# Optimization experiments

Hardware: AMD Instinct MI355X
Metric: run time of the kernel (lower is better)

The kernel has to match this reference:

```python
import jax, jax.numpy as jnp
import numpy as np
from jax import lax

PS = 8  # patch size

def setup_inputs() -> dict:
    key = jax.random.key(0)
    ks = jax.random.split(key, 7)
    dim = 64
    B, H, W = 4, 256, 256
    x = jax.random.normal(ks[0], (B, dim, H, W), dtype=jnp.float32)
    # to_hidden: Conv2d(dim, 6*dim, k=1)
    w_hidden = jax.random.normal(ks[1], (6 * dim, dim, 1, 1), dtype=jnp.float32) * 0.05
    b_hidden = jax.random.normal(ks[2], (6 * dim,), dtype=jnp.float32) * 0.01
    # to_hidden_dw: depthwise Conv2d(6*dim, 6*dim, k=3, pad=1, groups=6*dim)
    w_dw = jax.random.normal(ks[3], (6 * dim, 1, 3, 3), dtype=jnp.float32) * 0.05
    b_dw = jax.random.normal(ks[4], (6 * dim,), dtype=jnp.float32) * 0.01
    # project_out: Conv2d(2*dim, dim, k=1)
    w_out = jax.random.normal(ks[5], (dim, 2 * dim, 1, 1), dtype=jnp.float32) * 0.05
    b_out = jax.random.normal(ks[6], (dim,), dtype=jnp.float32) * 0.01
    return {"x": x, "w_hidden": w_hidden, "b_hidden": b_hidden,
            "w_dw": w_dw, "b_dw": b_dw, "w_out": w_out, "b_out": b_out}

def _conv(x, w, groups=1, padding='VALID'):
    return lax.conv_general_dilated(
        x, w, window_strides=(1, 1), padding=padding,
        dimension_numbers=('NCHW', 'OIHW', 'NCHW'),
        feature_group_count=groups)

def reference(x, w_hidden, b_hidden, w_dw, b_dw, w_out, b_out):
    # 1x1 expansion to 6*dim channels
    hidden = _conv(x, w_hidden) + b_hidden[None, :, None, None]
    # 3x3 depthwise conv (groups == channels)
    dw = _conv(hidden, w_dw, groups=w_dw.shape[0], padding='SAME') + b_dw[None, :, None, None]
    q, k, v = jnp.split(dw, 3, axis=1)  # each (B, 2*dim, H, W)
    B, C, H, W = q.shape
    # raw reshape into (B,C,H/8,W/8,8,8) exactly as torch .reshape on contiguous NCHW
    q_patch = q.reshape(B, C, H // PS, W // PS, PS, PS)
    k_patch = k.reshape(B, C, H // PS, W // PS, PS, PS)
    q_fft = jnp.fft.rfft2(q_patch)
    k_fft = jnp.fft.rfft2(k_patch)
    out = jnp.fft.irfft2(q_fft * k_fft, s=(PS, PS))  # circular conv of q,k patches
    out = out.reshape(B, C, (H // PS) * PS, (W // PS) * PS)
    output = v * out
    output = _conv(output, w_out) + b_out[None, :, None, None]
    return output
```

## Files before the change

kernel.cpp:

```cpp
#include <hip/hip_runtime.h>

#define HW 65536
#define W_IMG 256
#define H_IMG 256
#define CIN 64
#define CHID 384
#define CQK 128

__global__ __launch_bounds__(256) void k1_expand(
    const float* __restrict__ x_base,
    const float* __restrict__ wh,
    const float* __restrict__ bh,
    float* __restrict__ hidden_base,
    size_t x_bstride, size_t hid_bstride)
{
    const float* x = x_base + blockIdx.z * x_bstride;
    float* hidden  = hidden_base + blockIdx.z * hid_bstride;
    const int pxbase = blockIdx.x * 256;
    const int cobase = blockIdx.y * 48;
    const int tid  = threadIdx.x;
    const int lane = tid & 63;
    const int wq   = __builtin_amdgcn_readfirstlane(tid >> 6);
    const int px   = pxbase + lane * 4;
    const int cw   = cobase + wq * 12;

    float acc[12][4];
    #pragma unroll
    for (int i = 0; i < 12; ++i)
        #pragma unroll
        for (int j = 0; j < 4; ++j) acc[i][j] = 0.f;

    #pragma unroll 2
    for (int ci4 = 0; ci4 < CIN; ci4 += 4) {
        float4 xv[4];
        #pragma unroll
        for (int u = 0; u < 4; ++u)
            xv[u] = *reinterpret_cast<const float4*>(&x[(size_t)(ci4 + u) * HW + px]);
        #pragma unroll
        for (int i = 0; i < 12; ++i) {
            float4 wv = *reinterpret_cast<const float4*>(
                &wh[(size_t)(cw + i) * CIN + ci4]);
            float wu[4] = {wv.x, wv.y, wv.z, wv.w};
            #pragma unroll
            for (int u = 0; u < 4; ++u) {
                acc[i][0] += wu[u] * xv[u].x;
                acc[i][1] += wu[u] * xv[u].y;
                acc[i][2] += wu[u] * xv[u].z;
                acc[i][3] += wu[u] * xv[u].w;
            }
        }
    }

    #pragma unroll
    for (int i = 0; i < 12; ++i) {
        int co = cw + i;
        float b = bh[co];
        float4 o;
        o.x = acc[i][0] + b; o.y = acc[i][1] + b;
        o.z = acc[i][2] + b; o.w = acc[i][3] + b;
        *reinterpret_cast<float4*>(&hidden[(size_t)co * HW + px]) = o;
    }
}

#define QK_CH   2208
#define QK_ROW  276
#define QK_SEG  68
__global__ __launch_bounds__(256) void k2_fused(
    const float* __restrict__ hidden_base,
    const float* __restrict__ wdw,
    const float* __restrict__ bdw,
    float* __restrict__ vout_base,
    size_t hid_bstride, size_t vout_bstride)
{
    __shared__ float stg[10 * 264];
    __shared__ float qk[2 * QK_CH];

    const float* hidden = hidden_base + blockIdx.z * hid_bstride;
    float* vout         = vout_base + blockIdx.z * vout_bstride;

    const int c  = blockIdx.y;
    const int r0 = blockIdx.x * 8;
    const int tid = threadIdx.x;

    const int row = tid >> 5;
    const int seg = (tid >> 3) & 3;
    const int i   = tid & 7;
    const int gr  = r0 + row;
    const int wp0 = seg * 64 + i * 8;

    const float* hbv = hidden + (size_t)(c + 2 * CQK) * HW;
    float4 hv[3][2];
    float  hm[3], hp[3];
    #pragma unroll
    for (int ky = 0; ky < 3; ++ky) {
        int grr = gr + ky - 1;
        hv[ky][0] = make_float4(0.f, 0.f, 0.f, 0.f);
        hv[ky][1] = make_float4(0.f, 0.f, 0.f, 0.f);
        hm[ky] = 0.f; hp[ky] = 0.f;
        if ((unsigned)grr < H_IMG) {
            const float* rb = hbv + (size_t)grr * W_IMG;
            hv[ky][0] = *reinterpret_cast<const float4*>(&rb[wp0]);
            hv[ky][1] = *reinterpret_cast<const float4*>(&rb[wp0 + 4]);
            hm[ky] = (wp0 > 0)   ? rb[wp0 - 1] : 0.f;
            hp[ky] = (wp0 < 248) ? rb[wp0 + 8] : 0.f;
        }
    }

    const int w = tid;
    const int segw = w >> 6;
    const int tw   = w & 63;

    #pragma unroll
    for (int ch = 0; ch < 2; ++ch) {
        if (ch) __syncthreads();
        #pragma unroll
        for (int it = 0; it < 3; ++it) {
            int f4 = it * 256 + tid;
            if (f4 < 640) {
                int lr = f4 >> 6;
                int p4 = f4 & 63;
                int grr = r0 - 1 + lr;
                float4 v = make_float4(0.f, 0.f, 0.f, 0.f);
                if ((unsigned)grr < H_IMG)
                    v = *reinterpret_cast<const float4*>(
                        &hidden[(size_t)(c + ch * CQK) * HW + (size_t)grr * W_IMG + p4 * 4]);
                *reinterpret_cast<float4*>(&stg[lr * 264 + 4 + p4 * 4]) = v;
            }
        }
        if (tid < 10) {
            stg[tid * 264 + 3]   = 0.f;
            stg[tid * 264 + 260] = 0.f;
        }
        __syncthreads();

        const float* wv = wdw + (c + ch * CQK) * 9;
        const float bias = bdw[c + ch * CQK];
        const float w0 = wv[0], w1 = wv[1], w2 = wv[2];
        const float w3 = wv[3], w4 = wv[4], w5 = wv[5];
        const float w6 = wv[6], w7 = wv[7], w8 = wv[8];

        const float* S0 = &stg[w + 3];
        float am = S0[0],       a0 = S0[1],       ap = S0[2];
        float bm = S0[264],     b0 = S0[265],     bp = S0[266];
        #pragma unroll
        for (int r = 0; r < 8; ++r) {
            const float* Sr = S0 + (r + 2) * 264;
            float cm = Sr[0], c0 = Sr[1], cp = Sr[2];
            float a = bias + am * w0 + a0 * w1 + ap * w2
                           + bm * w3 + b0 * w4 + bp * w5
                           + cm * w6 + c0 * w7 + cp * w8;
            qk[ch * QK_CH + r * QK_ROW + segw * QK_SEG + tw] = a;
            am = bm; a0 = b0; ap = bp;
            bm = cm; b0 = c0; bp = cp;
        }
    }
    __syncthreads();

    const float* qb = &qk[row * QK_ROW + seg * QK_SEG];
    const float* kb = &qk[QK_CH + row * QK_ROW + seg * QK_SEG];

    float acc[8];
    #pragma unroll
    for (int j = 0; j < 8; ++j) acc[j] = 0.f;

    #pragma unroll
    for (int s = 0; s < 8; ++s) {
        int qr = (i - s) & 7;
        float4 ka = *reinterpret_cast<const float4*>(&kb[s * 8]);
        float4 kc = *reinterpret_cast<const float4*>(&kb[s * 8 + 4]);
        float4 qa = *reinterpret_cast<const float4*>(&qb[qr * 8]);
        float4 qc = *reinterpret_cast<const float4*>(&qb[qr * 8 + 4]);
        float kr[8] = {ka.x, ka.y, ka.z, ka.w, kc.x, kc.y, kc.z, kc.w};
        float qv[8] = {qa.x, qa.y, qa.z, qa.w, qc.x, qc.y, qc.z, qc.w};
        #pragma unroll
        for (int t = 0; t < 8; ++t)
            #pragma unroll
            for (int j = 0; j < 8; ++j)
                acc[j] += kr[t] * qv[(j - t) & 7];
    }

    const float* wvv = wdw + (c + 2 * CQK) * 9;
    const float vbias = bdw[c + 2 * CQK];
    float vc[8];
    #pragma unroll
    for (int j = 0; j < 8; ++j) vc[j] = vbias;
    #pragma unroll
    for (int ky = 0; ky < 3; ++ky) {
        float kw0 = wvv[ky * 3], kw1 = wvv[ky * 3 + 1], kw2 = wvv[ky * 3 + 2];
        float h[10];
        h[0] = hm[ky];
        h[1] = hv[ky][0].x; h[2] = hv[ky][0].y; h[3] = hv[ky][0].z; h[4] = hv[ky][0].w;
        h[5] = hv[ky][1].x; h[6] = hv[ky][1].y; h[7] = hv[ky][1].z; h[8] = hv[ky][1].w;
        h[9] = hp[ky];
        #pragma unroll
        for (int j = 0; j < 8; ++j)
            vc[j] += h[j] * kw0 + h[j + 1] * kw1 + h[j + 2] * kw2;
    }

    float* dst = &vout[(size_t)c * HW + (size_t)gr * W_IMG + wp0];
    float4 o0, o1;
    o0.x = acc[0] * vc[0]; o0.y = acc[1] * vc[1];
    o0.z = acc[2] * vc[2]; o0.w = acc[3] * vc[3];
    o1.x = acc[4] * vc[4]; o1.y = acc[5] * vc[5];
    o1.z = acc[6] * vc[6]; o1.w = acc[7] * vc[7];
    *reinterpret_cast<float4*>(dst)     = o0;
    *reinterpret_cast<float4*>(dst + 4) = o1;
}

__global__ __launch_bounds__(256) void k3_project(
    const float* __restrict__ vout_base,
    const float* __restrict__ wo,
    const float* __restrict__ bo,
    float* __restrict__ out_base,
    size_t vout_bstride, size_t out_bstride)
{
    const float* vout = vout_base + blockIdx.z * vout_bstride;
    float* out        = out_base + blockIdx.z * out_bstride;
    const int pxbase = blockIdx.x * 256;
    const int cobase = blockIdx.y * 16;
    const int tid  = threadIdx.x;
    const int lane = tid & 63;
    const int wq   = __builtin_amdgcn_readfirstlane(tid >> 6);
    const int px   = pxbase + lane * 4;
    const int cw   = cobase + wq * 4;

    float acc[4][4];
    #pragma unroll
    for (int i = 0; i < 4; ++i)
        #pragma unroll
        for (int j = 0; j < 4; ++j) acc[i][j] = 0.f;

    #pragma unroll 2
    for (int cc4 = 0; cc4 < CQK; cc4 += 4) {
        float4 xv[4];
        #pragma unroll
        for (int u = 0; u < 4; ++u)
            xv[u] = *reinterpret_cast<const float4*>(&vout[(size_t)(cc4 + u) * HW + px]);
        #pragma unroll
        for (int i = 0; i < 4; ++i) {
            float4 wv = *reinterpret_cast<const float4*>(
                &wo[(size_t)(cw + i) * CQK + cc4]);
            float wu[4] = {wv.x, wv.y, wv.z, wv.w};
            #pragma unroll
            for (int u = 0; u < 4; ++u) {
                acc[i][0] += wu[u] * xv[u].x;
                acc[i][1] += wu[u] * xv[u].y;
                acc[i][2] += wu[u] * xv[u].z;
                acc[i][3] += wu[u] * xv[u].w;
            }
        }
    }

    #pragma unroll
    for (int i = 0; i < 4; ++i) {
        int co = cw + i;
        float b = bo[co];
        float4 o;
        o.x = acc[i][0] + b; o.y = acc[i][1] + b;
        o.z = acc[i][2] + b; o.w = acc[i][3] + b;
        *reinterpret_cast<float4*>(&out[(size_t)co * HW + px]) = o;
    }
}

extern "C" void kernel_launch(void* const* d_in, const int* in_sizes, int n_in,
                              void* d_out, int out_size, void* d_ws, size_t ws_size,
                              hipStream_t stream) {
    const float* x   = (const float*)d_in[0];
    const float* wh  = (const float*)d_in[1];
    const float* bh  = (const float*)d_in[2];
    const float* wdw = (const float*)d_in[3];
    const float* bdw = (const float*)d_in[4];
    const float* wo  = (const float*)d_in[5];
    const float* bo  = (const float*)d_in[6];
    float* out = (float*)d_out;

    const size_t n_hid  = (size_t)CHID * HW;
    const size_t n_vout = (size_t)CQK * HW;
    const size_t n_x    = (size_t)CIN * HW;

    if (ws_size >= 4 * (n_hid + n_vout) * sizeof(float)) {
        float* hidden = (float*)d_ws;
        float* vout   = hidden + 4 * n_hid;
        k1_expand <<<dim3(HW / 256, CHID / 48, 4), 256, 0, stream>>>(
            x, wh, bh, hidden, n_x, n_hid);
        k2_fused  <<<dim3(H_IMG / 8, CQK, 4),      256, 0, stream>>>(
            hidden, wdw, bdw, vout, n_hid, n_vout);
        k3_project<<<dim3(HW / 256, 64 / 16, 4),   256, 0, stream>>>(
            vout, wo, bo, out, n_vout, n_x);
    } else {
        float* hidden = (float*)d_ws;
        float* vout   = hidden + n_hid;
        for (int b = 0; b < 4; ++b) {
            const float* xb = x + (size_t)b * n_x;
            float* ob       = out + (size_t)b * n_x;
            k1_expand <<<dim3(HW / 256, CHID / 48, 1), 256, 0, stream>>>(
                xb, wh, bh, hidden, 0, 0);
            k2_fused  <<<dim3(H_IMG / 8, CQK, 1),      256, 0, stream>>>(
                hidden, wdw, bdw, vout, 0, 0);
            k3_project<<<dim3(HW / 256, 64 / 16, 1),   256, 0, stream>>>(
                vout, wo, bo, ob, 0, 0);
        }
    }
}
```

Measured before the change: 403.8 us.

## Prefetch q/k tiles into registers upfront and split expand into two passes

In the fused depthwise/FFT kernel, the q and k halo tiles are now loaded from global memory into registers at kernel start, before the v loads, so all global reads are in flight together. The second channel's tile is then written to shared memory from registers instead of being fetched after a barrier. The expand kernel now computes its 12 output channels per wave as two passes of 6, which lowers accumulator register pressure but reloads the x inputs twice. The main costs are higher register use in k2 and extra x reads in k1.

```diff
diff --git a/kernel.cpp b/kernel.cpp
--- a/kernel.cpp
+++ b/kernel.cpp
@@ -22,43 +22,46 @@
     const int lane = tid & 63;
     const int wq   = __builtin_amdgcn_readfirstlane(tid >> 6);
     const int px   = pxbase + lane * 4;
-    const int cw   = cobase + wq * 12;
-
-    float acc[12][4];
-    #pragma unroll
-    for (int i = 0; i < 12; ++i)
-        #pragma unroll
-        for (int j = 0; j < 4; ++j) acc[i][j] = 0.f;
-
-    #pragma unroll 2
-    for (int ci4 = 0; ci4 < CIN; ci4 += 4) {
-        float4 xv[4];
-        #pragma unroll
-        for (int u = 0; u < 4; ++u)
-            xv[u] = *reinterpret_cast<const float4*>(&x[(size_t)(ci4 + u) * HW + px]);
-        #pragma unroll
-        for (int i = 0; i < 12; ++i) {
-            float4 wv = *reinterpret_cast<const float4*>(
-                &wh[(size_t)(cw + i) * CIN + ci4]);
-            float wu[4] = {wv.x, wv.y, wv.z, wv.w};
-            #pragma unroll
-            for (int u = 0; u < 4; ++u) {
-                acc[i][0] += wu[u] * xv[u].x;
-                acc[i][1] += wu[u] * xv[u].y;
-                acc[i][2] += wu[u] * xv[u].z;
-                acc[i][3] += wu[u] * xv[u].w;
+
+    #pragma unroll
+    for (int st = 0; st < 2; ++st) {
+        const int cw = cobase + st * 24 + wq * 6;
+        float acc[6][4];
+        #pragma unroll
+        for (int i = 0; i < 6; ++i)
+            #pragma unroll
+            for (int j = 0; j < 4; ++j) acc[i][j] = 0.f;
+
+        #pragma unroll 2
+        for (int ci4 = 0; ci4 < CIN; ci4 += 4) {
+            float4 xv[4];
+            #pragma unroll
+            for (int u = 0; u < 4; ++u)
+                xv[u] = *reinterpret_cast<const float4*>(&x[(size_t)(ci4 + u) * HW + px]);
+            #pragma unroll
+            for (int i = 0; i < 6; ++i) {
+                float4 wv = *reinterpret_cast<const float4*>(
+                    &wh[(size_t)(cw + i) * CIN + ci4]);
+                float wu[4] = {wv.x, wv.y, wv.z, wv.w};
+                #pragma unroll
+                for (int u = 0; u < 4; ++u) {
+                    acc[i][0] += wu[u] * xv[u].x;
+                    acc[i][1] += wu[u] * xv[u].y;
+                    acc[i][2] += wu[u] * xv[u].z;
+                    acc[i][3] += wu[u] * xv[u].w;
+                }
             }
         }
-    }
-
-    #pragma unroll
-    for (int i = 0; i < 12; ++i) {
-        int co = cw + i;
-        float b = bh[co];
-        float4 o;
-        o.x = acc[i][0] + b; o.y = acc[i][1] + b;
-        o.z = acc[i][2] + b; o.w = acc[i][3] + b;
-        *reinterpret_cast<float4*>(&hidden[(size_t)co * HW + px]) = o;
+
+        #pragma unroll
+        for (int i = 0; i < 6; ++i) {
+            int co = cw + i;
+            float b = bh[co];
+            float4 o;
+            o.x = acc[i][0] + b; o.y = acc[i][1] + b;
+            o.z = acc[i][2] + b; o.w = acc[i][3] + b;
+            *reinterpret_cast<float4*>(&hidden[(size_t)co * HW + px]) = o;
+        }
     }
 }
 
@@ -88,6 +91,46 @@
     const int gr  = r0 + row;
     const int wp0 = seg * 64 + i * 8;
 
+    float4 qreg[3];
+    #pragma unroll
+    for (int it = 0; it < 3; ++it) {
+        int f4 = it * 256 + tid;
+        qreg[it] = make_float4(0.f, 0.f, 0.f, 0.f);
+        if (f4 < 640) {
+            int lr = f4 >> 6, p4 = f4 & 63;
+            int grr = r0 - 1 + lr;
+            if ((unsigned)grr < H_IMG)
+                qreg[it] = *reinterpret_cast<const float4*>(
+                    &hidden[(size_t)c * HW + (size_t)grr * W_IMG + p4 * 4]);
+        }
+    }
+    float4 kreg[3];
+    #pragma unroll
+    for (int it = 0; it < 3; ++it) {
+        int f4 = it * 256 + tid;
+        kreg[it] = make_float4(0.f, 0.f, 0.f, 0.f);
+        if (f4 < 640) {
+            int lr = f4 >> 6, p4 = f4 & 63;
+            int grr = r0 - 1 + lr;
+            if ((unsigned)grr < H_IMG)
+                kreg[it] = *reinterpret_cast<const float4*>(
+                    &hidden[(size_t)(c + CQK) * HW + (size_t)grr * W_IMG + p4 * 4]);
+        }
+    }
+
+    #pragma unroll
+    for (int it = 0; it < 3; ++it) {
+        int f4 = it * 256 + tid;
+        if (f4 < 640) {
+            int lr = f4 >> 6, p4 = f4 & 63;
+            *reinterpret_cast<float4*>(&stg[lr * 264 + 4 + p4 * 4]) = qreg[it];
+        }
+    }
+    if (tid < 10) {
+        stg[tid * 264 + 3]   = 0.f;
+        stg[tid * 264 + 260] = 0.f;
+    }
+
     const float* hbv = hidden + (size_t)(c + 2 * CQK) * HW;
     float4 hv[3][2];
     float  hm[3], hp[3];
@@ -112,24 +155,16 @@
 
     #pragma unroll
     for (int ch = 0; ch < 2; ++ch) {
-        if (ch) __syncthreads();
-        #pragma unroll
-        for (int it = 0; it < 3; ++it) {
-            int f4 = it * 256 + tid;
-            if (f4 < 640) {
-                int lr = f4 >> 6;
-                int p4 = f4 & 63;
-                int grr = r0 - 1 + lr;
-                float4 v = make_float4(0.f, 0.f, 0.f, 0.f);
-                if ((unsigned)grr < H_IMG)
-                    v = *reinterpret_cast<const float4*>(
-                        &hidden[(size_t)(c + ch * CQK) * HW + (size_t)grr * W_IMG + p4 * 4]);
-                *reinterpret_cast<float4*>(&stg[lr * 264 + 4 + p4 * 4]) = v;
+        if (ch) {
+            __syncthreads();
+            #pragma unroll
+            for (int it = 0; it < 3; ++it) {
+                int f4 = it * 256 + tid;
+                if (f4 < 640) {
+                    int lr = f4 >> 6, p4 = f4 & 63;
+                    *reinterpret_cast<float4*>(&stg[lr * 264 + 4 + p4 * 4]) = kreg[it];
+                }
             }
-        }
-        if (tid < 10) {
-            stg[tid * 264 + 3]   = 0.f;
-            stg[tid * 264 + 260] = 0.f;
         }
         __syncthreads();
 
@@ -140,8 +175,8 @@
         const float w6 = wv[6], w7 = wv[7], w8 = wv[8];
 
         const float* S0 = &stg[w + 3];
-        float am = S0[0],       a0 = S0[1],       ap = S0[2];
-        float bm = S0[264],     b0 = S0[265],     bp = S0[266];
+        float am = S0[0],   a0 = S0[1],   ap = S0[2];
+        float bm = S0[264], b0 = S0[265], bp = S0[266];
         #pragma unroll
         for (int r = 0; r < 8; ++r) {
             const float* Sr = S0 + (r + 2) * 264;
```

New measurement: 432.6 us. 1.07x slower.
